# Performance work log

Hardware: AMD Instinct MI355X
Metric: run time of the kernel (lower is better)

Reference implementation:

```python
import jax, jax.numpy as jnp
import numpy as np

CH = 128

def _fir_kernel(ch, factor=2.0):
    # [1,3,3,1] outer product, normalized, scaled by factor**2 (== torch get_fir_kernel)
    k1 = jnp.array([1.0, 3.0, 3.0, 1.0], dtype=jnp.float32)
    k = jnp.outer(k1, k1)
    k = k / k.sum() * (factor ** 2)          # 4x4, sums to 4
    return jnp.tile(k[None, None], (ch, 1, 1, 1))  # (C,1,4,4) OIHW depthwise

def setup_inputs() -> dict:
    key = jax.random.key(0)
    x = jax.random.normal(key, (8, CH, 128, 128), dtype=jnp.float32)
    return {"x": x}

def reference(x) -> jnp.ndarray:
    B, C, H, W = x.shape
    k = _fir_kernel(C, factor=2.0)
    # torch F.conv_transpose2d(x, k, stride=2, padding=1, groups=C)
    # == forward conv with lhs_dilation=2, padding k-1-p=2 each side, spatially flipped kernel
    kf = k[:, :, ::-1, ::-1]  # symmetric kernel, flip for exactness
    out = jax.lax.conv_general_dilated(
        x, kf,
        window_strides=(1, 1),
        padding=((2, 2), (2, 2)),
        lhs_dilation=(2, 2),
        rhs_dilation=(1, 1),
        dimension_numbers=("NCHW", "OIHW", "NCHW"),
        feature_group_count=C,
    )
    # out shape: (B, C, 2H, 2W)
    return out
```

## Files before the change

### kernel.cpp

```cpp
#include <hip/hip_runtime.h>


#define IN_H 128
#define IN_W 128
#define ROWS_PER_WAVE 16

__global__ __launch_bounds__(512) void upsample_fir_kernel(
    const float* __restrict__ x, float* __restrict__ out) {
    const int lane = threadIdx.x & 63;
    const int wv   = threadIdx.x >> 6;
    const int bc   = blockIdx.x;
    const int iy0  = wv * ROWS_PER_WAVE;

    const float* xp = x + (size_t)bc * (IN_H * IN_W);
    const int OW = 2 * IN_W;
    float* op = out + (size_t)bc * (2 * IN_H) * OW + 4 * lane;

    const float2 z2 = make_float2(0.f, 0.f);

    float2 a = (iy0 > 0) ? ((const float2*)(xp + (iy0 - 1) * IN_W))[lane] : z2;
    float2 b = ((const float2*)(xp + iy0 * IN_W))[lane];

    #pragma unroll 4
    for (int iy = iy0; iy < iy0 + ROWS_PER_WAVE; ++iy) {
        const int ny = (iy + 1 < IN_H) ? (iy + 1) : (IN_H - 1);
        float2 cr = ((const float2*)(xp + ny * IN_W))[lane];
        float2 c;
        c.x = (iy + 1 < IN_H) ? cr.x : 0.f;
        c.y = (iy + 1 < IN_H) ? cr.y : 0.f;

        float2 t, u;
        t.x = (a.x + 3.f * b.x) * 0.25f;  u.x = (3.f * b.x + c.x) * 0.25f;
        t.y = (a.y + 3.f * b.y) * 0.25f;  u.y = (3.f * b.y + c.y) * 0.25f;

        float t_l = __shfl_up(t.y, 1);   if (lane == 0)  t_l = 0.f;
        float t_r = __shfl_down(t.x, 1); if (lane == 63) t_r = 0.f;
        float u_l = __shfl_up(u.y, 1);   if (lane == 0)  u_l = 0.f;
        float u_r = __shfl_down(u.x, 1); if (lane == 63) u_r = 0.f;

        float4 o, p;
        o.x = (t_l + 3.f * t.x) * 0.25f;
        o.y = (3.f * t.x + t.y) * 0.25f;
        o.z = (t.x + 3.f * t.y) * 0.25f;
        o.w = (3.f * t.y + t_r) * 0.25f;
        p.x = (u_l + 3.f * u.x) * 0.25f;
        p.y = (3.f * u.x + u.y) * 0.25f;
        p.z = (u.x + 3.f * u.y) * 0.25f;
        p.w = (3.f * u.y + u_r) * 0.25f;

        float* ob = op + (size_t)(2 * iy) * OW;
        *(float4*)(ob)      = o;
        *(float4*)(ob + OW) = p;

        a = b; b = c;
    }
}

extern "C" void kernel_launch(void* const* d_in, const int* in_sizes, int n_in,
                              void* d_out, int out_size, void* d_ws, size_t ws_size,
                              hipStream_t stream) {
    const float* x = (const float*)d_in[0];
    float* out = (float*)d_out;
    upsample_fir_kernel<<<8 * 128, 512, 0, stream>>>(x, out);
}
```

Before: 314.4 us.

## Split each image into 8-row strips, preload rows into registers, use FMA math

```diff
diff --git a/kernel.cpp b/kernel.cpp
--- a/kernel.cpp
+++ b/kernel.cpp
@@ -3,35 +3,41 @@
 
 #define IN_H 128
 #define IN_W 128
-#define ROWS_PER_WAVE 16
+#define ROWS 8
 
-__global__ __launch_bounds__(512) void upsample_fir_kernel(
+__global__ __launch_bounds__(256) void upsample_fir_kernel(
     const float* __restrict__ x, float* __restrict__ out) {
-    const int lane = threadIdx.x & 63;
-    const int wv   = threadIdx.x >> 6;
-    const int bc   = blockIdx.x;
-    const int iy0  = wv * ROWS_PER_WAVE;
+    const int lane  = threadIdx.x & 63;
+    const int wv    = threadIdx.x >> 6;
+    const int strip = blockIdx.x * 4 + wv;
+    const int bc    = strip >> 4;
+    const int iy0   = (strip & 15) * ROWS;
 
-    const float* xp = x + (size_t)bc * (IN_H * IN_W);
-    const int OW = 2 * IN_W;
-    float* op = out + (size_t)bc * (2 * IN_H) * OW + 4 * lane;
+    const float2* xr = (const float2*)(x + (size_t)bc * (IN_H * IN_W)) + lane;
 
     const float2 z2 = make_float2(0.f, 0.f);
+    float2 r[ROWS + 2];
 
-    float2 a = (iy0 > 0) ? ((const float2*)(xp + (iy0 - 1) * IN_W))[lane] : z2;
-    float2 b = ((const float2*)(xp + iy0 * IN_W))[lane];
+    r[0] = (iy0 > 0) ? xr[(iy0 - 1) * (IN_W / 2)] : z2;
+    #pragma unroll
+    for (int k = 0; k < ROWS + 1; ++k) {
+        const int ry = iy0 + k;
+        r[k + 1] = (ry < IN_H) ? xr[ry * (IN_W / 2)] : z2;
+    }
 
-    #pragma unroll 4
-    for (int iy = iy0; iy < iy0 + ROWS_PER_WAVE; ++iy) {
-        const int ny = (iy + 1 < IN_H) ? (iy + 1) : (IN_H - 1);
-        float2 cr = ((const float2*)(xp + ny * IN_W))[lane];
-        float2 c;
-        c.x = (iy + 1 < IN_H) ? cr.x : 0.f;
-        c.y = (iy + 1 < IN_H) ? cr.y : 0.f;
+    const int OW = 2 * IN_W;
+    float* ob = out + (size_t)bc * (2 * IN_H) * OW + (size_t)(2 * iy0) * OW
+              + 4 * lane;
+
+    const float s16 = 1.f / 16.f;
+
+    #pragma unroll
+    for (int k = 0; k < ROWS; ++k) {
+        const float2 A = r[k], B = r[k + 1], C = r[k + 2];
 
         float2 t, u;
-        t.x = (a.x + 3.f * b.x) * 0.25f;  u.x = (3.f * b.x + c.x) * 0.25f;
-        t.y = (a.y + 3.f * b.y) * 0.25f;  u.y = (3.f * b.y + c.y) * 0.25f;
+        t.x = fmaf(3.f, B.x, A.x);  t.y = fmaf(3.f, B.y, A.y);
+        u.x = fmaf(3.f, B.x, C.x);  u.y = fmaf(3.f, B.y, C.y);
 
         float t_l = __shfl_up(t.y, 1);   if (lane == 0)  t_l = 0.f;
         float t_r = __shfl_down(t.x, 1); if (lane == 63) t_r = 0.f;
@@ -39,20 +45,18 @@
         float u_r = __shfl_down(u.x, 1); if (lane == 63) u_r = 0.f;
 
         float4 o, p;
-        o.x = (t_l + 3.f * t.x) * 0.25f;
-        o.y = (3.f * t.x + t.y) * 0.25f;
-        o.z = (t.x + 3.f * t.y) * 0.25f;
-        o.w = (3.f * t.y + t_r) * 0.25f;
-        p.x = (u_l + 3.f * u.x) * 0.25f;
-        p.y = (3.f * u.x + u.y) * 0.25f;
-        p.z = (u.x + 3.f * u.y) * 0.25f;
-        p.w = (3.f * u.y + u_r) * 0.25f;
+        o.x = fmaf(3.f, t.x, t_l) * s16;
+        o.y = fmaf(3.f, t.x, t.y) * s16;
+        o.z = fmaf(3.f, t.y, t.x) * s16;
+        o.w = fmaf(3.f, t.y, t_r) * s16;
+        p.x = fmaf(3.f, u.x, u_l) * s16;
+        p.y = fmaf(3.f, u.x, u.y) * s16;
+        p.z = fmaf(3.f, u.y, u.x) * s16;
+        p.w = fmaf(3.f, u.y, u_r) * s16;
 
-        float* ob = op + (size_t)(2 * iy) * OW;
-        *(float4*)(ob)      = o;
-        *(float4*)(ob + OW) = p;
-
-        a = b; b = c;
+        float* orow = ob + (size_t)(2 * k) * OW;
+        *(float4*)(orow)      = o;
+        *(float4*)(orow + OW) = p;
     }
 }
 
@@ -61,5 +65,5 @@
                               hipStream_t stream) {
     const float* x = (const float*)d_in[0];
     float* out = (float*)d_out;
-    upsample_fir_kernel<<<8 * 128, 512, 0, stream>>>(x, out);
+    upsample_fir_kernel<<<4096, 256, 0, stream>>>(x, out);
 }
```

After: 307.3 us. 2.3% less time.
